# Kernel tuning notes

Measured on AMD Instinct MI355X. Metric: run time of the kernel, lower is better.

The kernel has to match this reference:

```python
import jax, jax.numpy as jnp
import numpy as np

H_SZ, W_SZ = 24, 24  # size for location=2 (H*W == N3)

def _ln(x, g, b, eps=1e-5):
    m = jnp.mean(x, axis=-1, keepdims=True)
    v = jnp.var(x, axis=-1, keepdims=True)
    return (x - m) / jnp.sqrt(v + eps) * g + b

def _cross_attn(value, x2, Wp, bp):
    # key = softmax(x2^T, dim=1) == softmax over channels; query = softmax over tokens
    k = jax.nn.softmax(x2, axis=2)   # [B,M,C], softmax over C
    q = jax.nn.softmax(x2, axis=1)   # [B,M,C], softmax over M
    ctx = jnp.einsum('bnc,bmc->bnm', value, k)   # value @ key
    att = jnp.einsum('bnm,bmc->bnc', ctx, q)     # context @ query
    return att @ Wp.T + bp

def _dwconv(x, Wdw, bdw, Hh, Ww):
    B, N, C = x.shape
    t = x.transpose(0, 2, 1).reshape(B, C, Hh, Ww)
    y = jax.lax.conv_general_dilated(t, Wdw, (1, 1), 'SAME',
                                     feature_group_count=C,
                                     dimension_numbers=('NCHW', 'OIHW', 'NCHW'))
    y = y + bdw[None, :, None, None]
    return y.reshape(B, C, N).transpose(0, 2, 1)

def setup_inputs() -> dict:
    key = jax.random.key(0)
    ks = jax.random.split(key, 16)
    B = 4; d0, d1, d2 = 128, 256, 512
    N1, N2, N3 = 96 * 96, 48 * 48, 24 * 24
    s = 0.02
    dh = 4 * d2
    inp = {}
    inp['x']  = jax.random.normal(ks[0], (B, N1, d0), jnp.float32)
    inp['x2'] = jax.random.normal(ks[1], (B, N2, d1), jnp.float32)
    inp['x3'] = jax.random.normal(ks[2], (B, N3, d2), jnp.float32)
    inp['W_lin']  = jax.random.normal(ks[3], (d2, d0)) * s   # linear: d0->d2
    inp['W_lin2'] = jax.random.normal(ks[4], (d2, d1)) * s   # linear2: d1->d2
    inp['W_lin3'] = jax.random.normal(ks[5], (d1, d0)) * s   # linear3: d0->d1
    inp['W_lin4'] = jax.random.normal(ks[6], (d2, d1)) * s   # linear4: d1->d2
    inp['w'] = jnp.ones((1,), jnp.float32)
    inp['Wp1'] = jax.random.normal(ks[7], (d2, d2)) * s;  inp['bp1'] = jnp.zeros((d2,))
    inp['Wp2'] = jax.random.normal(ks[8], (d2, d2)) * s;  inp['bp2'] = jnp.zeros((d2,))
    inp['Wp3'] = jax.random.normal(ks[9], (d1, d1)) * s;  inp['bp3'] = jnp.zeros((d1,))
    inp['Wp4'] = jax.random.normal(ks[10], (d2, d2)) * s; inp['bp4'] = jnp.zeros((d2,))
    inp['g_norm'] = jnp.ones((d2,)); inp['b_norm'] = jnp.zeros((d2,))
    inp['Wfc1'] = jax.random.normal(ks[11], (dh, d2)) * s; inp['bfc1'] = jnp.zeros((dh,))
    inp['Wdw']  = jax.random.normal(ks[12], (dh, 1, 3, 3)) * s; inp['bdw'] = jnp.zeros((dh,))
    inp['g_ln1'] = jnp.ones((dh,)); inp['b_ln1'] = jnp.zeros((dh,))
    inp['Wfc2'] = jax.random.normal(ks[13], (d2, dh)) * s; inp['bfc2'] = jnp.zeros((d2,))
    return inp

def reference(x, x2, x3, W_lin, W_lin2, W_lin3, W_lin4, w,
              Wp1, bp1, Wp2, bp2, Wp3, bp3, Wp4, bp4,
              g_norm, b_norm, Wfc1, bfc1, Wdw, bdw, g_ln1, b_ln1, Wfc2, bfc2):
    # location == 2 branch
    image  = x  @ W_lin.T    # [B,N1,d2]
    image2 = x2 @ W_lin2.T   # [B,N2,d2]
    image4 = x  @ W_lin3.T   # [B,N1,d1]
    atten1 = _cross_attn(x3, image,  Wp1, bp1)
    atten2 = _cross_attn(x3, image2, Wp2, bp2)
    a3 = _cross_attn(x2, image4, Wp3, bp3)   # [B,N2,d1]
    a3 = a3 @ W_lin4.T                        # [B,N2,d2]
    atten3 = _cross_attn(x3, a3, Wp4, bp4)    # [B,N3,d2]
    f = jax.nn.sigmoid(w)
    other = (1.0 - f) / 2.0
    atten_ = f * atten3 + other * atten2 + other * atten1
    atten = x3 + atten_
    an = _ln(atten, g_norm, b_norm)
    # MixFFN_skip (fc1 computed once; torch computes it twice with same result)
    h = an @ Wfc1.T + bfc1
    dw = _dwconv(h, Wdw, bdw, H_SZ, W_SZ)
    ax = jax.nn.gelu(_ln(dw + h, g_ln1, b_ln1), approximate=False)
    out = ax @ Wfc2.T + bfc2
    return atten + out
```

## Files before the change

kernel.cpp:

```cpp
#include <hip/hip_runtime.h>
#include <hip/hip_bf16.h>
#include <math.h>

typedef long long i64;
typedef __attribute__((ext_vector_type(8))) short short8v;
typedef __attribute__((ext_vector_type(4))) float float4v;

#define SPITCH 72
#define NCV 13

__device__ __forceinline__ float ldv(const void* p, i64 idx, int isBf16) {
  return isBf16 ? __bfloat162float(((const __hip_bfloat16*)p)[idx])
                : ((const float*)p)[idx];
}
__device__ __forceinline__ unsigned short bf16bits(float f) {
  __hip_bfloat16 h = __float2bfloat16(f);
  return *(unsigned short*)&h;
}
__device__ __forceinline__ float bits2f(unsigned short u) {
  union { unsigned int ui; float fl; } cv; cv.ui = ((unsigned int)u) << 16;
  return cv.fl;
}

__global__ void detect_dtype(const unsigned short* w, int* dt) {
  dt[0] = (w[0] == 0) ? 0 : 1;
}

struct CvArgs {
  const void* src[NCV];
  unsigned short* dst[NCV];
  i64 n[NCV];
  int blkStart[NCV + 1];
};
__global__ __launch_bounds__(256) void convert_many(const int* dt, CvArgs a) {
  int au = dt[0];
  int bid = blockIdx.x;
  int lo = 0;
  #pragma unroll
  for (int i = 0; i < NCV; ++i) if (bid >= a.blkStart[i + 1]) lo = i + 1;
  const void* s = a.src[lo];
  unsigned short* d = a.dst[lo];
  i64 n = a.n[lo];
  i64 base = ((i64)(bid - a.blkStart[lo]) * 256 + threadIdx.x) * 4;
  if (base + 4 <= n) {
    #pragma unroll
    for (int j = 0; j < 4; ++j) d[base + j] = bf16bits(ldv(s, base + j, au));
  } else {
    for (; base < n; ++base) d[base] = bf16bits(ldv(s, base, au));
  }
}

__global__ void transpose_dw(const int* dt, const void* Wdw, unsigned short* Wdwt) {
  int au = dt[0];
  int i = blockIdx.x * 256 + threadIdx.x;
  if (i >= 9 * 2048) return;
  int k = i / 2048, ch = i % 2048;
  Wdwt[i] = bf16bits(ldv(Wdw, (i64)ch * 9 + k, au));
}

__global__ __launch_bounds__(256) void gemm_mfma_bt(
    const int* dt,
    const unsigned short* A, i64 bsA,
    const unsigned short* Bt, i64 bsB,
    const void* bias, int biasDt,
    const void* add, int addDt, i64 bsAdd,
    void* C, i64 bsC, int outMode,
    int M, int N, int K, int flags,
    const void* wPtr, int alphaMode,
    float* csP, float* rsP)
{
  __shared__ unsigned short Ash[64 * SPITCH];
  __shared__ unsigned short Bsh[64 * SPITCH];
  __shared__ unsigned short LT[64 * SPITCH];

  const int au = dt[0];
  const int bDt = (biasDt == 2) ? au : biasDt;
  const int aDt = (addDt == 2) ? au : addDt;

  const int b  = blockIdx.z;
  const int m0 = blockIdx.y * 64;
  const int n0 = blockIdx.x * 64;
  const int t = threadIdx.x;
  const int lane = t & 63, wave = t >> 6;
  const int wr = (wave >> 1) * 32, wc = (wave & 1) * 32;
  const int quad = lane >> 4, l15 = lane & 15;
  const unsigned short* Ab = A + (i64)b * bsA;
  const unsigned short* Bb = Bt + (i64)b * bsB;
  const int sr = t >> 3, sg = (t & 7) * 8;

  float alpha = 1.0f;
  if (alphaMode) {
    float w0 = ldv(wPtr, 0, au);
    float f = 1.0f / (1.0f + expf(-w0));
    alpha = (alphaMode == 2) ? f : (1.0f - f) * 0.5f;
  }

  float4v acc00 = {0.f,0.f,0.f,0.f}, acc01 = {0.f,0.f,0.f,0.f};
  float4v acc10 = {0.f,0.f,0.f,0.f}, acc11 = {0.f,0.f,0.f,0.f};

  for (int k0 = 0; k0 < K; k0 += 64) {
    #pragma unroll
    for (int p = 0; p < 2; ++p) {
      int rr = sr + p * 32;
      *(short8v*)&Ash[rr * SPITCH + sg] = *(const short8v*)&Ab[(i64)(m0 + rr) * K + k0 + sg];
      *(short8v*)&Bsh[rr * SPITCH + sg] = *(const short8v*)&Bb[(i64)(n0 + rr) * K + k0 + sg];
    }
    __syncthreads();
    #pragma unroll
    for (int ks = 0; ks < 2; ++ks) {
      int ko = ks * 32 + quad * 8;
      short8v a0 = *(const short8v*)&Ash[(wr + l15) * SPITCH + ko];
      short8v a1 = *(const short8v*)&Ash[(wr + 16 + l15) * SPITCH + ko];
      short8v b0 = *(const short8v*)&Bsh[(wc + l15) * SPITCH + ko];
      short8v b1 = *(const short8v*)&Bsh[(wc + 16 + l15) * SPITCH + ko];
      acc00 = __builtin_amdgcn_mfma_f32_16x16x32_bf16(a0, b0, acc00, 0, 0, 0);
      acc01 = __builtin_amdgcn_mfma_f32_16x16x32_bf16(a0, b1, acc01, 0, 0, 0);
      acc10 = __builtin_amdgcn_mfma_f32_16x16x32_bf16(a1, b0, acc10, 0, 0, 0);
      acc11 = __builtin_amdgcn_mfma_f32_16x16x32_bf16(a1, b1, acc11, 0, 0, 0);
    }
    __syncthreads();
  }

  float* Cf = (float*)C;
  unsigned short* Ch = (unsigned short*)C;

  if (outMode == 2) {
    #pragma unroll
    for (int rg = 0; rg < 4; ++rg) {
      #pragma unroll
      for (int sub = 0; sub < 4; ++sub) {
        int lr = wr + quad * 4 + rg + (sub >> 1) * 16;
        int lc = wc + l15 + (sub & 1) * 16;
        float v = (sub == 0 ? acc00[rg] : sub == 1 ? acc01[rg] :
                   sub == 2 ? acc10[rg] : acc11[rg]) * alpha;
        if (bias) v += ldv(bias, n0 + lc, bDt);
        if (flags & 1) v = expf(v);
        LT[lc * SPITCH + lr] = bf16bits(v);
      }
    }
    __syncthreads();
    #pragma unroll
    for (int p = 0; p < 2; ++p) {
      int rr = sr + p * 32;
      short8v vv = *(short8v*)&LT[rr * SPITCH + sg];
      *(short8v*)(Ch + (i64)b * bsC + (i64)(n0 + rr) * M + m0 + sg) = vv;
    }
    if (csP) {
      if (t < 64) {
        const unsigned short* Lr = &LT[t * SPITCH];
        float s = 0.f;
        #pragma unroll
        for (int i = 0; i < 64; ++i) s += bits2f(Lr[i]);
        atomicAdd(&csP[(i64)b * N + n0 + t], s);
      } else if (t < 128) {
        int tok = t - 64;
        float s = 0.f;
        #pragma unroll
        for (int i = 0; i < 64; ++i) s += bits2f(LT[i * SPITCH + tok]);
        atomicAdd(&rsP[(i64)b * M + m0 + tok], s);
      }
    }
    return;
  }

  #pragma unroll
  for (int rg = 0; rg < 4; ++rg) {
    #pragma unroll
    for (int sub = 0; sub < 4; ++sub) {
      int lr = wr + quad * 4 + rg + (sub >> 1) * 16;
      int lc = wc + l15 + (sub & 1) * 16;
      int gi = m0 + lr, gj = n0 + lc;
      float v = (sub == 0 ? acc00[rg] : sub == 1 ? acc01[rg] :
                 sub == 2 ? acc10[rg] : acc11[rg]) * alpha;
      if (bias) v += ldv(bias, gj, bDt);
      if (add)  v += ldv(add, (i64)b * bsAdd + (i64)gi * N + gj, aDt);
      i64 idx = (i64)b * bsC + (i64)gi * N + gj;
      if (flags & 2) v += Cf[idx];
      if (flags & 1) v = expf(v);
      if (outMode == 1) Ch[idx] = bf16bits(v);
      else              Cf[idx] = v;
    }
  }
}

__global__ __launch_bounds__(256, 2) void softprod128_db(
    const unsigned short* Gt, const float* rs, float* Sraw,
    int C, i64 M, int splits, int mChunk, int nPairs)
{
  __shared__ unsigned short Ash[2][128 * SPITCH];
  __shared__ unsigned short Bsh[2][128 * SPITCH];

  const int bid = blockIdx.x;
  const int xcd = bid & 7;
  const int q = bid >> 3;
  const int gHi = q / nPairs;
  const int pr = q - gHi * nPairs;
  const int g = gHi * 8 + xcd;
  const int b  = g / splits;
  const int sp = g - b * splits;

  const int nStrips = C >> 7;
  int rem = pr, s0 = 0;
  while (rem >= nStrips - s0) { rem -= nStrips - s0; ++s0; }
  const int s1 = s0 + rem;
  const int c0 = s0 * 128;
  const int c1 = s1 * 128;

  const int t = threadIdx.x;
  const int lane = t & 63, wave = t >> 6;
  const int wrow = (wave >> 1) * 64, wcol = (wave & 1) * 64;
  const int quad = lane >> 4, l15 = lane & 15;
  const unsigned short* Gb = Gt + (i64)b * C * M;
  const float* rib = rs + (i64)b * M;
  const int sg = (t & 7) * 8;
  const int r4 = t >> 3;

  float4v acc[4][4];
  #pragma unroll
  for (int i = 0; i < 4; ++i)
    #pragma unroll
    for (int j = 0; j < 4; ++j)
      acc[i][j] = (float4v){0.f, 0.f, 0.f, 0.f};

  const i64 mBeg = (i64)sp * mChunk;
  const int nt = mChunk >> 6;

  const unsigned short* Arow = &Gb[(i64)(c0 + r4) * M + sg];
  const unsigned short* Brow = &Gb[(i64)(c1 + r4) * M + sg];

  short8v pa[4], pb[4];
  float rv[8];

  auto loadF = [&](i64 m0) {
    #pragma unroll
    for (int pp = 0; pp < 4; ++pp) {
      pa[pp] = *(const short8v*)&Arow[(i64)32 * pp * M + m0];
      pb[pp] = *(const short8v*)&Brow[(i64)32 * pp * M + m0];
    }
    #pragma unroll
    for (int j = 0; j < 8; ++j) {
      float r_ = rsqrtf(rib[m0 + sg + j]);
      rv[j] = r_ * r_;
    }
  };
  auto stageF = [&](int bi) {
    #pragma unroll
    for (int pp = 0; pp < 4; ++pp) {
      *(short8v*)&Ash[bi][(r4 + 32 * pp) * SPITCH + sg] = pa[pp];
      short8v sb;
      #pragma unroll
      for (int j = 0; j < 8; ++j)
        sb[j] = (short)bf16bits(bits2f((unsigned short)pb[pp][j]) * rv[j]);
      *(short8v*)&Bsh[bi][(r4 + 32 * pp) * SPITCH + sg] = sb;
    }
  };
  auto mfmaF = [&](int bi) {
    #pragma unroll
    for (int ks = 0; ks < 2; ++ks) {
      int ko = ks * 32 + quad * 8;
      short8v af[4], bfr[4];
      #pragma unroll
      for (int i = 0; i < 4; ++i) {
        af[i]  = *(const short8v*)&Ash[bi][(wrow + i * 16 + l15) * SPITCH + ko];
        bfr[i] = *(const short8v*)&Bsh[bi][(wcol + i * 16 + l15) * SPITCH + ko];
      }
      #pragma unroll
      for (int i = 0; i < 4; ++i)
        #pragma unroll
        for (int j = 0; j < 4; ++j)
          acc[i][j] = __builtin_amdgcn_mfma_f32_16x16x32_bf16(af[i], bfr[j], acc[i][j], 0, 0, 0);
    }
  };

  loadF(mBeg);

  int cur = 0;
  for (int tt = 0; tt < nt; ++tt) {
    stageF(cur);
    __syncthreads();
    if (tt + 1 < nt) loadF(mBeg + (i64)(tt + 1) * 64);
    mfmaF(cur);
    cur ^= 1;
  }

  float* Sb = Sraw + (i64)b * C * C;
  #pragma unroll
  for (int i = 0; i < 4; ++i)
    #pragma unroll
    for (int rg = 0; rg < 4; ++rg) {
      int r = c0 + wrow + i * 16 + quad * 4 + rg;
      #pragma unroll
      for (int j = 0; j < 4; ++j) {
        int cc = c1 + wcol + j * 16 + l15;
        atomicAdd(&Sb[(i64)r * C + cc], acc[i][j][rg]);
      }
    }
}

__global__ void scale_S_sym_bf16(const float* Sraw, const float* cs,
                                 unsigned short* Sb, int C, i64 total) {
  i64 i = (i64)blockIdx.x * blockDim.x + threadIdx.x;
  if (i >= total) return;
  i64 cc2 = (i64)C * C;
  i64 b = i / cc2;
  i64 r = (i % cc2) / C;
  int cp = (int)(i % C);
  const float* Sb_ = Sraw + b * cc2;
  float v = (((int)r >> 6) <= (cp >> 6)) ? Sb_[r * C + cp] : Sb_[(i64)cp * C + r];
  Sb[i] = bf16bits(v / cs[b * C + cp]);
}

__global__ __launch_bounds__(256) void transpose_to_bf16(
    const float* T, unsigned short* Tt, int Nn) {
  __shared__ float tile[64][65];
  int b = blockIdx.z;
  int i0 = blockIdx.y * 64, j0 = blockIdx.x * 64;
  const float* Tb = T + (i64)b * Nn * Nn;
  unsigned short* Ttb = Tt + (i64)b * Nn * Nn;
  int t = threadIdx.x;
  int li = t >> 6, lj = t & 63;
  #pragma unroll
  for (int p = 0; p < 16; ++p)
    tile[li + p * 4][lj] = Tb[(i64)(i0 + li + p * 4) * Nn + j0 + lj];
  __syncthreads();
  #pragma unroll
  for (int p = 0; p < 16; ++p) {
    int row = li + p * 4;
    Ttb[(i64)(j0 + row) * Nn + i0 + lj] = bf16bits(tile[lj][row]);
  }
}

__global__ void combine_bias(const int* dt, const void* w, const void* bp1,
                             const void* bp2, const void* bp4, float* biasc) {
  int au = dt[0];
  int j = threadIdx.x;
  float w0 = ldv(w, 0, au);
  float f = 1.0f / (1.0f + expf(-w0));
  float other = (1.0f - f) * 0.5f;
  biasc[j] = f * ldv(bp4, j, au) + other * (ldv(bp1, j, au) + ldv(bp2, j, au));
}

__global__ __launch_bounds__(256) void layernorm512(const int* dt, const float* X,
                                                    const void* g, const void* be,
                                                    __hip_bfloat16* Y) {
  int au = dt[0];
  i64 row = blockIdx.x;
  const float* xr = X + row * 512;
  int t = threadIdx.x;
  float x0 = xr[t], x1 = xr[t + 256];
  float s = x0 + x1, q = x0 * x0 + x1 * x1;
  #pragma unroll
  for (int off = 32; off; off >>= 1) { s += __shfl_down(s, off); q += __shfl_down(q, off); }
  __shared__ float ws_[4], wq_[4];
  int lane = t & 63, wv = t >> 6;
  if (!lane) { ws_[wv] = s; wq_[wv] = q; }
  __syncthreads();
  float S = ws_[0] + ws_[1] + ws_[2] + ws_[3];
  float Q = wq_[0] + wq_[1] + wq_[2] + wq_[3];
  float mean = S * (1.f / 512.f);
  float var = Q * (1.f / 512.f) - mean * mean;
  float inv = rsqrtf(var + 1e-5f);
  Y[row * 512 + t]       = __float2bfloat16((x0 - mean) * inv * ldv(g, t, au) + ldv(be, t, au));
  Y[row * 512 + t + 256] = __float2bfloat16((x1 - mean) * inv * ldv(g, t + 256, au) + ldv(be, t + 256, au));
}

__global__ __launch_bounds__(256) void dwconv_ln_gelu(
    const int* dt,
    const unsigned short* h, const unsigned short* Wdwt, const void* bdw,
    const void* g, const void* be, unsigned short* ax)
{
  int au = dt[0];
  int n = blockIdx.x;
  int b = blockIdx.y;
  int y = n / 24, x = n % 24;
  const unsigned short* hb = h + (i64)b * 576 * 2048;
  int t = threadIdx.x;
  int ch0 = t * 8;

  float accv[8];
  #pragma unroll
  for (int j = 0; j < 8; ++j) accv[j] = ldv(bdw, ch0 + j, au);

  #pragma unroll
  for (int dy = 0; dy < 3; ++dy) {
    int yy = y + dy - 1;
    if (yy < 0 || yy >= 24) continue;
    #pragma unroll
    for (int dx = 0; dx < 3; ++dx) {
      int xx = x + dx - 1;
      if (xx < 0 || xx >= 24) continue;
      short8v hv = *(const short8v*)&hb[(i64)(yy * 24 + xx) * 2048 + ch0];
      short8v wv = *(const short8v*)&Wdwt[(i64)(dy * 3 + dx) * 2048 + ch0];
      #pragma unroll
      for (int j = 0; j < 8; ++j)
        accv[j] += bits2f((unsigned short)hv[j]) * bits2f((unsigned short)wv[j]);
    }
  }

  short8v hc = *(const short8v*)&hb[(i64)n * 2048 + ch0];
  float z[8];
  float s = 0.f, q = 0.f;
  #pragma unroll
  for (int j = 0; j < 8; ++j) {
    float zz = accv[j] + bits2f((unsigned short)hc[j]);
    z[j] = zz; s += zz; q += zz * zz;
  }

  #pragma unroll
  for (int off = 32; off; off >>= 1) { s += __shfl_down(s, off); q += __shfl_down(q, off); }
  __shared__ float ws_[4], wq_[4];
  int lane = t & 63, wv2 = t >> 6;
  if (!lane) { ws_[wv2] = s; wq_[wv2] = q; }
  __syncthreads();
  float S = ws_[0] + ws_[1] + ws_[2] + ws_[3];
  float Q = wq_[0] + wq_[1] + wq_[2] + wq_[3];
  float mean = S * (1.f / 2048.f);
  float var = Q * (1.f / 2048.f) - mean * mean;
  float inv = rsqrtf(var + 1e-5f);

  short8v ov;
  #pragma unroll
  for (int j = 0; j < 8; ++j) {
    float v = (z[j] - mean) * inv * ldv(g, ch0 + j, au) + ldv(be, ch0 + j, au);
    float gl = 0.5f * v * (1.0f + erff(v * 0.70710678118654752f));
    ov[j] = (short)bf16bits(gl);
  }
  *(short8v*)&ax[((i64)b * 576 + n) * 2048 + ch0] = ov;
}

extern "C" void kernel_launch(void* const* d_in, const int* in_sizes, int n_in,
                              void* d_out, int out_size, void* d_ws, size_t ws_size,
                              hipStream_t stream) {
  const int B = 4, N1 = 9216, N2 = 2304, N3 = 576;
  const int d0 = 128, d1 = 256, d2 = 512, dh = 2048;

  const void* x     = d_in[0];
  const void* x2    = d_in[1];
  const void* x3    = d_in[2];
  const void* Wlin  = d_in[3];
  const void* Wlin2 = d_in[4];
  const void* Wlin3 = d_in[5];
  const void* Wlin4 = d_in[6];
  const void* w     = d_in[7];
  const void* Wp1 = d_in[8];  const void* bp1 = d_in[9];
  const void* Wp2 = d_in[10]; const void* bp2 = d_in[11];
  const void* Wp3 = d_in[12]; const void* bp3 = d_in[13];
  const void* Wp4 = d_in[14]; const void* bp4 = d_in[15];
  const void* gnorm = d_in[16]; const void* bnorm = d_in[17];
  const void* Wfc1 = d_in[18]; const void* bfc1 = d_in[19];
  const void* Wdw  = d_in[20]; const void* bdw  = d_in[21];
  const void* gln1 = d_in[22]; const void* bln1 = d_in[23];
  const void* Wfc2 = d_in[24]; const void* bfc2 = d_in[25];

  char* base = (char*)d_ws;
  size_t o = 0;
  auto alloc = [&](size_t n) -> char* {
    char* r = base + o; o += (n + 255) & ~(size_t)255; return r;
  };

  int* dtFlag = (int*)alloc(256);
  char* arena = alloc((size_t)B * N1 * d2 * 2);
  float* rsBig   = (float*)alloc((size_t)B * N1 * 4);
  float* rsSmall = (float*)alloc((size_t)B * N2 * 4);
  size_t csBytes = (size_t)B * (d2 + d2 + d1 + d2) * 4;
  float* csAll = (float*)alloc(csBytes);
  float* cs1  = csAll;
  float* cs2  = cs1 + B * d2;
  float* cs4  = cs2 + B * d2;
  float* cs3b = cs4 + B * d1;
  float* Sraw  = (float*)alloc((size_t)B * d2 * d2 * 4);
  float* S3raw = (float*)alloc((size_t)B * d1 * d1 * 4);
  unsigned short* Sb16  = (unsigned short*)alloc((size_t)B * d2 * d2 * 2);
  unsigned short* S3b16 = (unsigned short*)alloc((size_t)B * d1 * d1 * 2);
  unsigned short* U3t   = (unsigned short*)alloc((size_t)B * d1 * d1 * 2);
  float* T     = (float*)alloc((size_t)B * d2 * d2 * 4);
  float* biasc = (float*)alloc((size_t)d2 * 4);
  unsigned short* xb  = (unsigned short*)alloc((size_t)B * N1 * d0 * 2);
  unsigned short* x2b = (unsigned short*)alloc((size_t)B * N2 * d1 * 2);
  unsigned short* x3b = (unsigned short*)alloc((size_t)B * N3 * d2 * 2);
  unsigned short* Wlinb  = (unsigned short*)alloc((size_t)d2 * d0 * 2);
  unsigned short* Wlin2b = (unsigned short*)alloc((size_t)d2 * d1 * 2);
  unsigned short* Wlin3b = (unsigned short*)alloc((size_t)d1 * d0 * 2);
  unsigned short* Wlin4b = (unsigned short*)alloc((size_t)d2 * d1 * 2);
  unsigned short* Wp1b = (unsigned short*)alloc((size_t)d2 * d2 * 2);
  unsigned short* Wp2b = (unsigned short*)alloc((size_t)d2 * d2 * 2);
  unsigned short* Wp3b = (unsigned short*)alloc((size_t)d1 * d1 * 2);
  unsigned short* Wp4b = (unsigned short*)alloc((size_t)d2 * d2 * 2);
  unsigned short* Wfc1b = (unsigned short*)alloc((size_t)dh * d2 * 2);
  unsigned short* Wfc2b = (unsigned short*)alloc((size_t)d2 * dh * 2);
  unsigned short* Wdwt  = (unsigned short*)alloc((size_t)9 * dh * 2);

  unsigned short* Et1    = (unsigned short*)arena;
  unsigned short* Et4    = (unsigned short*)arena;
  unsigned short* a3buf  = (unsigned short*)(arena + 18874368);
  unsigned short* EtA3b  = (unsigned short*)arena;
  unsigned short* Et2    = (unsigned short*)arena;
  float*          atten  = (float*)arena;
  __hip_bfloat16* an     = (__hip_bfloat16*)(arena + 4718592);
  unsigned short* hbuf   = (unsigned short*)(arena + 7077888);
  unsigned short* axb    = (unsigned short*)(arena + 16515072);
  unsigned short* Tt     = (unsigned short*)(arena + 28573696);

  detect_dtype<<<dim3(1), dim3(1), 0, stream>>>((const unsigned short*)w, dtFlag);
  hipMemsetAsync(csAll, 0, csBytes, stream);

  {
    CvArgs a;
    const void* srcs[NCV] = { x, x2, x3, Wlin, Wlin2, Wlin3, Wlin4,
                              Wp1, Wp2, Wp3, Wp4, Wfc1, Wfc2 };
    unsigned short* dsts[NCV] = { xb, x2b, x3b, Wlinb, Wlin2b, Wlin3b, Wlin4b,
                                  Wp1b, Wp2b, Wp3b, Wp4b, Wfc1b, Wfc2b };
    i64 ns[NCV] = { (i64)B*N1*d0, (i64)B*N2*d1, (i64)B*N3*d2,
                    (i64)d2*d0, (i64)d2*d1, (i64)d1*d0, (i64)d2*d1,
                    (i64)d2*d2, (i64)d2*d2, (i64)d1*d1, (i64)d2*d2,
                    (i64)dh*d2, (i64)d2*dh };
    int cum = 0;
    for (int i = 0; i < NCV; ++i) {
      a.src[i] = srcs[i]; a.dst[i] = dsts[i]; a.n[i] = ns[i];
      a.blkStart[i] = cum;
      cum += (int)((ns[i] + 1023) / 1024);
    }
    a.blkStart[NCV] = cum;
    convert_many<<<dim3(cum), dim3(256), 0, stream>>>(dtFlag, a);
    transpose_dw<<<dim3((9 * dh + 255) / 256), dim3(256), 0, stream>>>(dtFlag, Wdw, Wdwt);
  }

  auto gemm64 = [&](const unsigned short* A_, i64 bsA,
                    const unsigned short* Bt_, i64 bsB,
                    const void* bias_, int biasDt,
                    const void* add_, int addDt, i64 bsAdd,
                    void* C_, i64 bsC, int outMode,
                    int M_, int N_, int K_, int flags, int alphaMode,
                    float* csP = nullptr, float* rsP = nullptr) {
    gemm_mfma_bt<<<dim3(N_ / 64, M_ / 64, B), dim3(256), 0, stream>>>(
        dtFlag, A_, bsA, Bt_, bsB, bias_, biasDt, add_, addDt, bsAdd,
        C_, bsC, outMode, M_, N_, K_, flags, w, alphaMode, csP, rsP);
  };

  auto softtail = [&](unsigned short* Et, float* cs, float* rsArr,
                      float* SrawB, unsigned short* SbB, int C, int M, int splits) {
    hipMemsetAsync(SrawB, 0, (size_t)B * C * C * 4, stream);
    int nStrips = C / 128;
    int nPairs = nStrips * (nStrips + 1) / 2;
    int nBlk = nPairs * B * splits;
    softprod128_db<<<dim3(nBlk), dim3(256), 0, stream>>>(
        Et, rsArr, SrawB, C, M, splits, M / splits, nPairs);
    i64 totS = (i64)B * C * C;
    scale_S_sym_bf16<<<dim3((unsigned)((totS + 255) / 256)), dim3(256), 0, stream>>>(
        SrawB, cs, SbB, C, totS);
  };

  hipMemsetAsync(rsBig, 0, (size_t)B * N1 * 4, stream);
  gemm64(xb, (i64)N1 * d0, Wlinb, 0, nullptr, 0, nullptr, 0, 0,
         Et1, (i64)N1 * d2, 2, N1, d2, d0, 1, 0, cs1, rsBig);
  softtail(Et1, cs1, rsBig, Sraw, Sb16, d2, N1, 12);
  gemm64(Sb16, (i64)d2 * d2, Wp1b, 0, nullptr, 0, nullptr, 0, 0,
         T, (i64)d2 * d2, 0, d2, d2, d2, 0, 1);

  hipMemsetAsync(rsBig, 0, (size_t)B * N1 * 4, stream);
  gemm64(xb, (i64)N1 * d0, Wlin3b, 0, nullptr, 0, nullptr, 0, 0,
         Et4, (i64)N1 * d1, 2, N1, d1, d0, 1, 0, cs4, rsBig);
  softtail(Et4, cs4, rsBig, S3raw, S3b16, d1, N1, 36);
  gemm64(S3b16, (i64)d1 * d1, Wp3b, 0, nullptr, 0, nullptr, 0, 0,
         U3t, (i64)d1 * d1, 2, d1, d1, d1, 0, 0);
  gemm64(x2b, (i64)N2 * d1, U3t, (i64)d1 * d1, bp3, 2, nullptr, 0, 0,
         a3buf, (i64)N2 * d1, 1, N2, d1, d1, 0, 0);
  hipMemsetAsync(rsSmall, 0, (size_t)B * N2 * 4, stream);
  gemm64(a3buf, (i64)N2 * d1, Wlin4b, 0, nullptr, 0, nullptr, 0, 0,
         EtA3b, (i64)N2 * d2, 2, N2, d2, d1, 1, 0, cs3b, rsSmall);
  softtail(EtA3b, cs3b, rsSmall, Sraw, Sb16, d2, N2, 12);
  gemm64(Sb16, (i64)d2 * d2, Wp4b, 0, nullptr, 0, nullptr, 0, 0,
         T, (i64)d2 * d2, 0, d2, d2, d2, 2, 2);

  hipMemsetAsync(rsSmall, 0, (size_t)B * N2 * 4, stream);
  gemm64(x2b, (i64)N2 * d1, Wlin2b, 0, nullptr, 0, nullptr, 0, 0,
         Et2, (i64)N2 * d2, 2, N2, d2, d1, 1, 0, cs2, rsSmall);
  softtail(Et2, cs2, rsSmall, Sraw, Sb16, d2, N2, 12);
  gemm64(Sb16, (i64)d2 * d2, Wp2b, 0, nullptr, 0, nullptr, 0, 0,
         T, (i64)d2 * d2, 0, d2, d2, d2, 2, 1);

  transpose_to_bf16<<<dim3(d2 / 64, d2 / 64, B), dim3(256), 0, stream>>>(T, Tt, d2);
  combine_bias<<<dim3(1), dim3(d2), 0, stream>>>(dtFlag, w, bp1, bp2, bp4, biasc);

  gemm64(x3b, (i64)N3 * d2, Tt, (i64)d2 * d2, biasc, 0, x3, 2, (i64)N3 * d2,
         atten, (i64)N3 * d2, 0, N3, d2, d2, 0, 0);

  layernorm512<<<dim3(B * N3), dim3(256), 0, stream>>>(dtFlag, atten, gnorm, bnorm, an);

  gemm64((const unsigned short*)an, (i64)N3 * d2, Wfc1b, 0, bfc1, 2, nullptr, 0, 0,
         hbuf, (i64)N3 * dh, 1, N3, dh, d2, 0, 0);

  dwconv_ln_gelu<<<dim3(N3, B), dim3(256), 0, stream>>>(
      dtFlag, hbuf, Wdwt, bdw, gln1, bln1, axb);

  gemm64(axb, (i64)N3 * dh, Wfc2b, 0, bfc2, 2,
         atten, 0, (i64)N3 * d2,
         d_out, (i64)N3 * d2, 0, N3, d2, dh, 0, 0);

  (void)in_sizes; (void)n_in; (void)out_size; (void)ws_size;
}
```

Before: 557.1 us.

## Replace atomic split-K reduction with partial tile buffers reduced in scale kernel

The split-M symmetric product kernel now writes each 128x128 tile's partial sums with plain stores into a per-split partial buffer, instead of atomically adding into a zeroed C×C matrix. The scale/symmetrize kernel then sums the partials across splits, maps each element to its upper-triangle tile, and converts to bf16. This removes the per-softtail memsets and the global float atomics. In exchange, every split's partial tiles are written and read back, which adds memory traffic proportional to the split count.

```diff
diff --git a/kernel.cpp b/kernel.cpp
--- a/kernel.cpp
+++ b/kernel.cpp
@@ -184,8 +184,8 @@
 }
 
 __global__ __launch_bounds__(256, 2) void softprod128_db(
-    const unsigned short* Gt, const float* rs, float* Sraw,
-    int C, i64 M, int splits, int mChunk, int nPairs)
+    const unsigned short* Gt, const float* rs, float* Part,
+    int C, i64 M, int splits, int mChunk, int nPairs, int Bn)
 {
   __shared__ unsigned short Ash[2][128 * SPITCH];
   __shared__ unsigned short Bsh[2][128 * SPITCH];
@@ -283,31 +283,39 @@
     cur ^= 1;
   }
 
-  float* Sb = Sraw + (i64)b * C * C;
+  float* Pb = Part + (((i64)sp * Bn + b) * nPairs + pr) * 16384;
   #pragma unroll
   for (int i = 0; i < 4; ++i)
     #pragma unroll
     for (int rg = 0; rg < 4; ++rg) {
-      int r = c0 + wrow + i * 16 + quad * 4 + rg;
+      int rr = wrow + i * 16 + quad * 4 + rg;
       #pragma unroll
       for (int j = 0; j < 4; ++j) {
-        int cc = c1 + wcol + j * 16 + l15;
-        atomicAdd(&Sb[(i64)r * C + cc], acc[i][j][rg]);
+        int cc = wcol + j * 16 + l15;
+        Pb[rr * 128 + cc] = acc[i][j][rg];
       }
     }
 }
 
-__global__ void scale_S_sym_bf16(const float* Sraw, const float* cs,
-                                 unsigned short* Sb, int C, i64 total) {
+__global__ __launch_bounds__(256) void scale_S_part_bf16(
+    const float* Part, const float* cs, unsigned short* Sb,
+    int C, int nStrips, int splits, int nPairs, int Bn, i64 total) {
   i64 i = (i64)blockIdx.x * blockDim.x + threadIdx.x;
   if (i >= total) return;
   i64 cc2 = (i64)C * C;
-  i64 b = i / cc2;
-  i64 r = (i % cc2) / C;
+  int b  = (int)(i / cc2);
+  int r  = (int)((i % cc2) / C);
   int cp = (int)(i % C);
-  const float* Sb_ = Sraw + b * cc2;
-  float v = (((int)r >> 6) <= (cp >> 6)) ? Sb_[r * C + cp] : Sb_[(i64)cp * C + r];
-  Sb[i] = bf16bits(v / cs[b * C + cp]);
+  int R = r >> 7, Cp = cp >> 7;
+  int a = R < Cp ? R : Cp, b2 = R < Cp ? Cp : R;
+  int idx = a * nStrips - (a * (a - 1)) / 2 + (b2 - a);
+  int row = (R <= Cp ? r : cp) & 127;
+  int col = (R <= Cp ? cp : r) & 127;
+  const float* base = Part + ((i64)b * nPairs + idx) * 16384 + row * 128 + col;
+  i64 stride = (i64)Bn * nPairs * 16384;
+  float v = 0.f;
+  for (int sp = 0; sp < splits; ++sp) v += base[(i64)sp * stride];
+  Sb[i] = bf16bits(v / cs[(i64)b * C + cp]);
 }
 
 __global__ __launch_bounds__(256) void transpose_to_bf16(
@@ -468,8 +476,7 @@
   float* cs2  = cs1 + B * d2;
   float* cs4  = cs2 + B * d2;
   float* cs3b = cs4 + B * d1;
-  float* Sraw  = (float*)alloc((size_t)B * d2 * d2 * 4);
-  float* S3raw = (float*)alloc((size_t)B * d1 * d1 * 4);
+  float* Part = (float*)alloc((size_t)12 * B * 10 * 16384 * 4);
   unsigned short* Sb16  = (unsigned short*)alloc((size_t)B * d2 * d2 * 2);
   unsigned short* S3b16 = (unsigned short*)alloc((size_t)B * d1 * d1 * 2);
   unsigned short* U3t   = (unsigned short*)alloc((size_t)B * d1 * d1 * 2);
@@ -538,29 +545,28 @@
   };
 
   auto softtail = [&](unsigned short* Et, float* cs, float* rsArr,
-                      float* SrawB, unsigned short* SbB, int C, int M, int splits) {
-    hipMemsetAsync(SrawB, 0, (size_t)B * C * C * 4, stream);
+                      unsigned short* SbB, int C, int M, int splits) {
     int nStrips = C / 128;
     int nPairs = nStrips * (nStrips + 1) / 2;
     int nBlk = nPairs * B * splits;
     softprod128_db<<<dim3(nBlk), dim3(256), 0, stream>>>(
-        Et, rsArr, SrawB, C, M, splits, M / splits, nPairs);
+        Et, rsArr, Part, C, M, splits, M / splits, nPairs, B);
     i64 totS = (i64)B * C * C;
-    scale_S_sym_bf16<<<dim3((unsigned)((totS + 255) / 256)), dim3(256), 0, stream>>>(
-        SrawB, cs, SbB, C, totS);
+    scale_S_part_bf16<<<dim3((unsigned)((totS + 255) / 256)), dim3(256), 0, stream>>>(
+        Part, cs, SbB, C, nStrips, splits, nPairs, B, totS);
   };
 
   hipMemsetAsync(rsBig, 0, (size_t)B * N1 * 4, stream);
   gemm64(xb, (i64)N1 * d0, Wlinb, 0, nullptr, 0, nullptr, 0, 0,
          Et1, (i64)N1 * d2, 2, N1, d2, d0, 1, 0, cs1, rsBig);
-  softtail(Et1, cs1, rsBig, Sraw, Sb16, d2, N1, 12);
+  softtail(Et1, cs1, rsBig, Sb16, d2, N1, 12);
   gemm64(Sb16, (i64)d2 * d2, Wp1b, 0, nullptr, 0, nullptr, 0, 0,
          T, (i64)d2 * d2, 0, d2, d2, d2, 0, 1);
 
   hipMemsetAsync(rsBig, 0, (size_t)B * N1 * 4, stream);
   gemm64(xb, (i64)N1 * d0, Wlin3b, 0, nullptr, 0, nullptr, 0, 0,
          Et4, (i64)N1 * d1, 2, N1, d1, d0, 1, 0, cs4, rsBig);
-  softtail(Et4, cs4, rsBig, S3raw, S3b16, d1, N1, 36);
+  softtail(Et4, cs4, rsBig, S3b16, d1, N1, 36);
   gemm64(S3b16, (i64)d1 * d1, Wp3b, 0, nullptr, 0, nullptr, 0, 0,
          U3t, (i64)d1 * d1, 2, d1, d1, d1, 0, 0);
   gemm64(x2b, (i64)N2 * d1, U3t, (i64)d1 * d1, bp3, 2, nullptr, 0, 0,
@@ -568,14 +574,14 @@
   hipMemsetAsync(rsSmall, 0, (size_t)B * N2 * 4, stream);
   gemm64(a3buf, (i64)N2 * d1, Wlin4b, 0, nullptr, 0, nullptr, 0, 0,
          EtA3b, (i64)N2 * d2, 2, N2, d2, d1, 1, 0, cs3b, rsSmall);
-  softtail(EtA3b, cs3b, rsSmall, Sraw, Sb16, d2, N2, 12);
+  softtail(EtA3b, cs3b, rsSmall, Sb16, d2, N2, 12);
   gemm64(Sb16, (i64)d2 * d2, Wp4b, 0, nullptr, 0, nullptr, 0, 0,
          T, (i64)d2 * d2, 0, d2, d2, d2, 2, 2);
 
   hipMemsetAsync(rsSmall, 0, (size_t)B * N2 * 4, stream);
   gemm64(x2b, (i64)N2 * d1, Wlin2b, 0, nullptr, 0, nullptr, 0, 0,
          Et2, (i64)N2 * d2, 2, N2, d2, d1, 1, 0, cs2, rsSmall);
-  softtail(Et2, cs2, rsSmall, Sraw, Sb16, d2, N2, 12);
+  softtail(Et2, cs2, rsSmall, Sb16, d2, N2, 12);
   gemm64(Sb16, (i64)d2 * d2, Wp2b, 0, nullptr, 0, nullptr, 0, 0,
          T, (i64)d2 * d2, 0, d2, d2, d2, 2, 1);
 
```

Result: slower. 608.7 us (+9.2%).
